# Kernel tuning notes

Hardware: AMD Instinct MI355X
Metric: run time of the kernel (lower is better)

## Reference

```python
import jax, jax.numpy as jnp
import numpy as np

BN_EPS = 1e-5

def _bn_relu(x, gamma, beta):
    # training-mode BatchNorm1d: biased batch stats over (B, N) per channel
    mean = x.mean(axis=(0, 2), keepdims=True)
    var = x.var(axis=(0, 2), keepdims=True)
    xn = (x - mean) * jax.lax.rsqrt(var + BN_EPS)
    return jax.nn.relu(xn * gamma[None, :, None] + beta[None, :, None])


def setup_inputs() -> dict:
    key = jax.random.key(0)
    ks = jax.random.split(key, 12)
    B, n1, n2, c1, c2 = 16, 4096, 1024, 128, 256
    in_ch, mlp = c1 + c2, [256, 128]
    xyz1 = jax.random.uniform(ks[0], (B, n1, 3), dtype=jnp.float32)
    xyz2 = jax.random.uniform(ks[1], (B, n2, 3), dtype=jnp.float32)
    feat1 = jax.random.normal(ks[2], (B, c1, n1), dtype=jnp.float32)
    feat2 = jax.random.normal(ks[3], (B, c2, n2), dtype=jnp.float32)
    # Conv1d(k=1) weights as (out, in) matrices; kaiming-ish scale
    w0 = jax.random.normal(ks[4], (mlp[0], in_ch), dtype=jnp.float32) / np.sqrt(in_ch)
    b0 = jnp.zeros((mlp[0],), jnp.float32)
    g0 = jnp.ones((mlp[0],), jnp.float32)
    be0 = jnp.zeros((mlp[0],), jnp.float32)
    w1 = jax.random.normal(ks[5], (mlp[1], mlp[0]), dtype=jnp.float32) / np.sqrt(mlp[0])
    b1 = jnp.zeros((mlp[1],), jnp.float32)
    g1 = jnp.ones((mlp[1],), jnp.float32)
    be1 = jnp.zeros((mlp[1],), jnp.float32)
    return {"xyz1": xyz1, "xyz2": xyz2, "feat1": feat1, "feat2": feat2,
            "w0": w0, "b0": b0, "g0": g0, "be0": be0,
            "w1": w1, "b1": b1, "g1": g1, "be1": be1}


def reference(xyz1, xyz2, feat1, feat2, w0, b0, g0, be0, w1, b1, g1, be1):
    # three_nn_interpolate: squared pairwise dists (B, n1, n2)
    d = jnp.sum((xyz1[:, :, None, :] - xyz2[:, None, :, :]) ** 2, axis=-1)
    neg_d3, idx3 = jax.lax.top_k(-d, 3)          # 3 smallest dists
    d3 = -neg_d3                                  # (B, n1, 3)
    w = 1.0 / (d3 + 1e-8)
    w = w / jnp.sum(w, axis=-1, keepdims=True)
    # gather feat2 at knn indices: (B, c2, n1, 3)
    gathered = jnp.take_along_axis(feat2[:, :, None, :], idx3[:, None, :, :], axis=3)
    interp = jnp.sum(gathered * w[:, None, :, :], axis=-1)  # (B, c2, n1)

    x = jnp.concatenate([feat1, interp], axis=1)            # (B, c1+c2, n1)
    x = _bn_relu(jnp.einsum('oc,bcn->bon', w0, x) + b0[None, :, None], g0, be0)
    x = _bn_relu(jnp.einsum('oc,bcn->bon', w1, x) + b1[None, :, None], g1, be1)
    return x
```

## Files before the change

kernel.cpp:

```cpp
#include <hip/hip_runtime.h>
#include <hip/hip_bf16.h>

typedef unsigned short u16;
typedef __attribute__((ext_vector_type(8))) __bf16 bf16x8;
typedef __attribute__((ext_vector_type(4))) float floatx4;

#define B_   16
#define N1_  4096
#define N2_  1024
#define C1_  128
#define C2_  256
#define CIN_ 384
#define CM_  256
#define CO_  128

__device__ __forceinline__ u16 f2bf(float f) {
  unsigned u = __float_as_uint(f);
  u = (u + 0x7fffu + ((u >> 16) & 1u)) >> 16;
  return (u16)u;
}
__device__ __forceinline__ float bf2f(u16 h) {
  return __uint_as_float(((unsigned)h) << 16);
}

union U128 { uint4 u; bf16x8 v; u16 s[8]; };

__device__ __forceinline__ bf16x8 ldfrag(const u16* p) {
  U128 x; x.u = *(const uint4*)p; return x.v;
}
__device__ __forceinline__ uint4 pack8(const u16* h) {
  uint4 u;
  u.x = (unsigned)h[0] | ((unsigned)h[1] << 16);
  u.y = (unsigned)h[2] | ((unsigned)h[3] << 16);
  u.z = (unsigned)h[4] | ((unsigned)h[5] << 16);
  u.w = (unsigned)h[6] | ((unsigned)h[7] << 16);
  return u;
}


__global__ __launch_bounds__(256) void knn_part_kernel(
    const float* __restrict__ xyz1, const float* __restrict__ xyz2,
    float* __restrict__ pd, int* __restrict__ pi,
    const float* __restrict__ w0, const float* __restrict__ w1,
    u16* __restrict__ w0b, u16* __restrict__ w1b)
{
  __shared__ float4 sp[128];
  int t = threadIdx.x;
  if (blockIdx.x == 16) {
    int item = (blockIdx.y * 8 + blockIdx.z) * 256 + t;
    if (item < 12288) {
      int m = item / 48, kc = item % 48;
      const float* p = w0 + m * CIN_ + kc * 8;
      u16 h8[8];
      #pragma unroll
      for (int j = 0; j < 8; ++j) h8[j] = f2bf(p[j]);
      int mt = m >> 4, col = m & 15, kt = kc >> 2, quad = kc & 3;
      *(uint4*)(w0b + ((mt*12 + kt)*512 + (quad*16 + col)*8)) = pack8(h8);
    } else if (item < 16384) {
      int i2 = item - 12288;
      int m = i2 >> 5, kc = i2 & 31;
      const float* p = w1 + m * CM_ + kc * 8;
      u16 h8[8];
      #pragma unroll
      for (int j = 0; j < 8; ++j) h8[j] = f2bf(p[j]);
      int mt = m >> 4, col = m & 15, kt = kc >> 2, quad = kc & 3;
      *(uint4*)(w1b + ((mt*8 + kt)*512 + (quad*16 + col)*8)) = pack8(h8);
    }
    return;
  }
  int b = blockIdx.y, chunk = blockIdx.z;
  const float* p2 = xyz2 + ((size_t)b * N2_ + chunk * 128) * 3;
  if (t < 128) sp[t] = make_float4(p2[t*3], p2[t*3+1], p2[t*3+2], 0.f);
  __syncthreads();
  int i = blockIdx.x * 256 + t;
  const float* p1 = xyz1 + ((size_t)b * N1_ + i) * 3;
  float x = p1[0], y = p1[1], z = p1[2];
  float d0 = 1e30f, d1 = 1e30f, d2 = 1e30f;
  int i0 = 0, i1 = 0, i2 = 0;
  int jb = chunk * 128;
  #pragma unroll 4
  for (int j = 0; j < 128; ++j) {
    float4 p = sp[j];
    float dx = x - p.x, dy = y - p.y, dz = z - p.z;
    float d = dx*dx + dy*dy + dz*dz;
    if (d < d2) {
      int jj = jb + j;
      if (d < d0)      { d2=d1; i2=i1; d1=d0; i1=i0; d0=d; i0=jj; }
      else if (d < d1) { d2=d1; i2=i1; d1=d;  i1=jj; }
      else             { d2=d;  i2=jj; }
    }
  }
  int o = chunk*65536 + b*4096 + i;
  pd[o] = d0; pd[o + 524288] = d1; pd[o + 1048576] = d2;
  pi[o] = i0; pi[o + 524288] = i1; pi[o + 1048576] = i2;
}

__global__ __launch_bounds__(256) void knn_merge_kernel(
    const float* __restrict__ pd, const int* __restrict__ pi,
    int* __restrict__ idx_out, float* __restrict__ w_out)
{
  int p = blockIdx.x * 256 + threadIdx.x;
  float d0 = 1e30f, d1 = 1e30f, d2 = 1e30f;
  int i0 = 0, i1 = 0, i2 = 0;
  #pragma unroll
  for (int c = 0; c < 8; ++c) {
    int o = c*65536 + p;
    #pragma unroll
    for (int k = 0; k < 3; ++k) {
      float d = pd[o + k*524288];
      int ix = pi[o + k*524288];
      if (d < d2) {
        if (d < d0)      { d2=d1; i2=i1; d1=d0; i1=i0; d0=d; i0=ix; }
        else if (d < d1) { d2=d1; i2=i1; d1=d;  i1=ix; }
        else             { d2=d;  i2=ix; }
      }
    }
  }
  float w0 = 1.f/(d0+1e-8f), w1 = 1.f/(d1+1e-8f), w2 = 1.f/(d2+1e-8f);
  float inv = 1.f/(w0+w1+w2);
  idx_out[p]          = i0;
  idx_out[p +  65536] = i1;
  idx_out[p + 131072] = i2;
  w_out[p]            = w0*inv;
  w_out[p +  65536]   = w1*inv;
  w_out[p + 131072]   = w2*inv;
}

__global__ __launch_bounds__(256) void tr2_kernel(
    const float* __restrict__ feat2, u16* __restrict__ feat2Tb)
{
  __shared__ float sA[64][257];
  int b = blockIdx.y;
  int n0 = blockIdx.x * 64;
  int t = threadIdx.x;
  #pragma unroll
  for (int j = 0; j < 16; ++j) {
    int flat4 = t + j * 256;
    int c = flat4 >> 4, nn4 = (flat4 & 15) * 4;
    float4 v = *(const float4*)(feat2 + ((size_t)b*C2_ + c)*N2_ + n0 + nn4);
    sA[nn4+0][c] = v.x; sA[nn4+1][c] = v.y; sA[nn4+2][c] = v.z; sA[nn4+3][c] = v.w;
  }
  __syncthreads();
  int nn = t & 63, chunk = t >> 6;
  u16* dst = feat2Tb + ((size_t)b*N2_ + n0 + nn)*C2_ + chunk*64;
  #pragma unroll
  for (int g = 0; g < 8; ++g) {
    u16 h8[8];
    #pragma unroll
    for (int j = 0; j < 8; ++j) h8[j] = f2bf(sA[nn][chunk*64 + g*8 + j]);
    *(uint4*)(dst + g*8) = pack8(h8);
  }
}

__global__ __launch_bounds__(256) void prep_fused_kernel(
    const float* __restrict__ feat1, const u16* __restrict__ feat2Tb,
    const int* __restrict__ idx_in, const float* __restrict__ w_in,
    u16* __restrict__ xcatT)
{
  __shared__ float sA[64][133];
  int b = blockIdx.y;
  int t = threadIdx.x;
  if (blockIdx.x < 64) {
    int n0 = blockIdx.x * 64;
    #pragma unroll
    for (int j = 0; j < 8; ++j) {
      int flat4 = t + j * 256;
      int c = flat4 >> 4, nn4 = (flat4 & 15) * 4;
      float4 v = *(const float4*)(feat1 + ((size_t)b*C1_ + c)*N1_ + n0 + nn4);
      sA[nn4+0][c] = v.x; sA[nn4+1][c] = v.y; sA[nn4+2][c] = v.z; sA[nn4+3][c] = v.w;
    }
    __syncthreads();
    int nn = t & 63, chunk = t >> 6;
    int n = n0 + nn, nt = n >> 4, col = n & 15;
    u16* tb = xcatT + ((size_t)b*256 + nt)*12*512;
    #pragma unroll
    for (int g = 0; g < 4; ++g) {
      int c0 = chunk*32 + g*8;
      u16 h8[8];
      #pragma unroll
      for (int j = 0; j < 8; ++j) h8[j] = f2bf(sA[nn][c0 + j]);
      *(uint4*)(tb + (size_t)chunk*512 + (g*16 + col)*8) = pack8(h8);
    }
  } else {
    int p0 = (blockIdx.x - 64) * 64;
    int seg = t & 31;
    int pl  = t >> 5;
    #pragma unroll 2
    for (int pass = 0; pass < 8; ++pass) {
      int n = p0 + pass*8 + pl;
      int base = b*N1_ + n;
      int i0 = idx_in[base], i1 = idx_in[base + 65536], i2 = idx_in[base + 131072];
      float w0 = w_in[base], w1 = w_in[base + 65536], w2 = w_in[base + 131072];
      const u16* fb = feat2Tb + (size_t)b*N2_*C2_ + seg*8;
      U128 a, c, d;
      a.u = *(const uint4*)(fb + (size_t)i0*C2_);
      c.u = *(const uint4*)(fb + (size_t)i1*C2_);
      d.u = *(const uint4*)(fb + (size_t)i2*C2_);
      u16 h8[8];
      #pragma unroll
      for (int j = 0; j < 8; ++j)
        h8[j] = f2bf(w0*bf2f(a.s[j]) + w1*bf2f(c.s[j]) + w2*bf2f(d.s[j]));
      int nt = n >> 4, col = n & 15;
      int kt = 4 + (seg >> 2), quad = seg & 3;
      *(uint4*)(xcatT + (((size_t)b*256 + nt)*12 + kt)*512 + (quad*16 + col)*8) = pack8(h8);
    }
  }
}

__global__ __launch_bounds__(256) void gemm1_mfma(
    const u16* __restrict__ xcatT, const u16* __restrict__ w0b,
    const float* __restrict__ b0p, u16* __restrict__ y0T,
    float* __restrict__ p0)
{
  __shared__ float ps[4][64][2];
  int t = threadIdx.x;
  int wave = t >> 6, lane = t & 63;
  int col = lane & 15, quad = lane >> 4;
  int wm = wave >> 1, wn = wave & 1;
  int b = blockIdx.y;
  int mtb = blockIdx.z*8 + wm*4;
  int ntb = blockIdx.x*8 + wn*4;

  const u16* ap = w0b + lane*8;
  const u16* bp = xcatT + ((size_t)(b*256 + ntb)*12)*512 + lane*8;

  floatx4 acc[4][4] = {};
  bf16x8 af[4], bf[4], afn[4], bfn[4];
  #pragma unroll
  for (int i = 0; i < 4; ++i) {
    af[i] = ldfrag(ap + (size_t)((mtb+i)*12)*512);
    bf[i] = ldfrag(bp + (size_t)(i*12)*512);
  }
  #pragma unroll 1
  for (int kt = 1; kt < 12; ++kt) {
    #pragma unroll
    for (int i = 0; i < 4; ++i) afn[i] = ldfrag(ap + (size_t)((mtb+i)*12 + kt)*512);
    #pragma unroll
    for (int i = 0; i < 4; ++i) bfn[i] = ldfrag(bp + (size_t)(i*12 + kt)*512);
    #pragma unroll
    for (int mt = 0; mt < 4; ++mt)
      #pragma unroll
      for (int nt = 0; nt < 4; ++nt)
        acc[mt][nt] = __builtin_amdgcn_mfma_f32_16x16x32_bf16(af[mt], bf[nt], acc[mt][nt], 0, 0, 0);
    #pragma unroll
    for (int i = 0; i < 4; ++i) { af[i] = afn[i]; bf[i] = bfn[i]; }
  }
  #pragma unroll
  for (int mt = 0; mt < 4; ++mt)
    #pragma unroll
    for (int nt = 0; nt < 4; ++nt)
      acc[mt][nt] = __builtin_amdgcn_mfma_f32_16x16x32_bf16(af[mt], bf[nt], acc[mt][nt], 0, 0, 0);

  int m0 = blockIdx.z*128 + wm*64;
  #pragma unroll
  for (int mt = 0; mt < 4; ++mt) {
    float4 bias4 = *(const float4*)(b0p + m0 + mt*16 + quad*4);
    float bia[4] = {bias4.x, bias4.y, bias4.z, bias4.w};
    int kt_out = (m0 >> 5) + (mt >> 1);
    int quad_out = ((mt & 1) << 1) | (quad >> 1);
    int j0 = (quad & 1) * 4;
    float s[4] = {}, q[4] = {};
    #pragma unroll
    for (int nt = 0; nt < 4; ++nt) {
      int nt_g = ntb + nt;
      u16 h[4];
      #pragma unroll
      for (int r = 0; r < 4; ++r) {
        float v = acc[mt][nt][r] + bia[r];
        u16 hh = f2bf(v);
        float vr = bf2f(hh);
        h[r] = hh; s[r] += vr; q[r] += vr*vr;
      }
      *(ushort4*)(y0T + (((size_t)b*256 + nt_g)*8 + kt_out)*512 + (quad_out*16 + col)*8 + j0)
          = make_ushort4(h[0], h[1], h[2], h[3]);
    }
    #pragma unroll
    for (int r = 0; r < 4; ++r) {
      float ss = s[r], qq = q[r];
      #pragma unroll
      for (int msk = 1; msk < 16; msk <<= 1) { ss += __shfl_xor(ss, msk); qq += __shfl_xor(qq, msk); }
      if (col == 0) {
        ps[wave][mt*16 + quad*4 + r][0] = ss;
        ps[wave][mt*16 + quad*4 + r][1] = qq;
      }
    }
  }
  __syncthreads();
  {
    int c = t >> 1, k = t & 1;
    int wbase = (c >> 6) * 2, ch = c & 63;
    float v = ps[wbase][ch][k] + ps[wbase+1][ch][k];
    size_t l = (size_t)blockIdx.z*512 + blockIdx.y*32 + blockIdx.x;
    p0[l*256 + t] = v;
  }
}

__global__ __launch_bounds__(256) void stats_kernel(
    const float* __restrict__ p, const float* __restrict__ g,
    const float* __restrict__ be, float* __restrict__ scale,
    float* __restrict__ shift, int half_split)
{
  int c = blockIdx.x, t = threadIdx.x;
  size_t base = half_split ? ((size_t)(c >> 7) * 512 * 256 + (size_t)(c & 127) * 2)
                           : ((size_t)c * 2);
  float s = 0.f, q = 0.f;
  #pragma unroll
  for (int i = 0; i < 2; ++i) {
    float2 v = *(const float2*)(p + base + (size_t)(t + i*256) * 256);
    s += v.x; q += v.y;
  }
  #pragma unroll
  for (int m = 1; m < 64; m <<= 1) { s += __shfl_xor(s, m); q += __shfl_xor(q, m); }
  __shared__ float2 red[4];
  if ((t & 63) == 0) red[t >> 6] = make_float2(s, q);
  __syncthreads();
  if (t == 0) {
    float ss = red[0].x + red[1].x + red[2].x + red[3].x;
    float qq = red[0].y + red[1].y + red[2].y + red[3].y;
    float mu  = ss * (1.f/65536.f);
    float var = qq * (1.f/65536.f) - mu*mu;
    float a = g[c] * rsqrtf(var + 1e-5f);
    scale[c] = a; shift[c] = be[c] - mu*a;
  }
}

__global__ __launch_bounds__(256) void gemm2_mfma(
    const u16* __restrict__ y0T, const u16* __restrict__ w1b,
    const float* __restrict__ b1p,
    const float* __restrict__ scale0, const float* __restrict__ shift0,
    float* __restrict__ out, float* __restrict__ p1)
{
  __shared__ float a0s[CM_], bb0s[CM_];
  __shared__ float ps[4][64][2];
  int t = threadIdx.x;
  a0s[t] = scale0[t]; bb0s[t] = shift0[t];
  __syncthreads();
  int wave = t >> 6, lane = t & 63;
  int col = lane & 15, quad = lane >> 4;
  int wm = wave >> 1, wn = wave & 1;
  int b = blockIdx.y;
  int mtb = wm*4;
  int ntb = blockIdx.x*8 + wn*4;

  const u16* ap = w1b + lane*8;
  const u16* bp = y0T + ((size_t)(b*256 + ntb)*8)*512 + lane*8;

  floatx4 acc[4][4] = {};
  bf16x8 af[4], afn[4];
  U128 braw[4], brawn[4];
  #pragma unroll
  for (int i = 0; i < 4; ++i) {
    af[i] = ldfrag(ap + (size_t)((mtb+i)*8)*512);
    braw[i].u = *(const uint4*)(bp + (size_t)(i*8)*512);
  }
  #pragma unroll 1
  for (int kt = 1; kt < 8; ++kt) {
    #pragma unroll
    for (int i = 0; i < 4; ++i) afn[i] = ldfrag(ap + (size_t)((mtb+i)*8 + kt)*512);
    #pragma unroll
    for (int i = 0; i < 4; ++i) brawn[i].u = *(const uint4*)(bp + (size_t)(i*8 + kt)*512);
    int c0 = (kt-1)*32 + quad*8;
    float4 av0 = *(const float4*)&a0s[c0], av1 = *(const float4*)&a0s[c0+4];
    float4 bv0 = *(const float4*)&bb0s[c0], bv1 = *(const float4*)&bb0s[c0+4];
    float av[8] = {av0.x,av0.y,av0.z,av0.w,av1.x,av1.y,av1.z,av1.w};
    float bv[8] = {bv0.x,bv0.y,bv0.z,bv0.w,bv1.x,bv1.y,bv1.z,bv1.w};
    bf16x8 bfv[4];
    #pragma unroll
    for (int i = 0; i < 4; ++i) {
      u16 h8[8];
      #pragma unroll
      for (int j = 0; j < 8; ++j)
        h8[j] = f2bf(fmaxf(fmaf(bf2f(braw[i].s[j]), av[j], bv[j]), 0.f));
      U128 x; x.u = pack8(h8); bfv[i] = x.v;
    }
    #pragma unroll
    for (int mt = 0; mt < 4; ++mt)
      #pragma unroll
      for (int nt = 0; nt < 4; ++nt)
        acc[mt][nt] = __builtin_amdgcn_mfma_f32_16x16x32_bf16(af[mt], bfv[nt], acc[mt][nt], 0, 0, 0);
    #pragma unroll
    for (int i = 0; i < 4; ++i) { af[i] = afn[i]; braw[i] = brawn[i]; }
  }
  {
    int c0 = 7*32 + quad*8;
    float4 av0 = *(const float4*)&a0s[c0], av1 = *(const float4*)&a0s[c0+4];
    float4 bv0 = *(const float4*)&bb0s[c0], bv1 = *(const float4*)&bb0s[c0+4];
    float av[8] = {av0.x,av0.y,av0.z,av0.w,av1.x,av1.y,av1.z,av1.w};
    float bv[8] = {bv0.x,bv0.y,bv0.z,bv0.w,bv1.x,bv1.y,bv1.z,bv1.w};
    bf16x8 bfv[4];
    #pragma unroll
    for (int i = 0; i < 4; ++i) {
      u16 h8[8];
      #pragma unroll
      for (int j = 0; j < 8; ++j)
        h8[j] = f2bf(fmaxf(fmaf(bf2f(braw[i].s[j]), av[j], bv[j]), 0.f));
      U128 x; x.u = pack8(h8); bfv[i] = x.v;
    }
    #pragma unroll
    for (int mt = 0; mt < 4; ++mt)
      #pragma unroll
      for (int nt = 0; nt < 4; ++nt)
        acc[mt][nt] = __builtin_amdgcn_mfma_f32_16x16x32_bf16(af[mt], bfv[nt], acc[mt][nt], 0, 0, 0);
  }

  int m0 = wm*64;
  int n0 = blockIdx.x*128 + wn*64;
  #pragma unroll
  for (int mt = 0; mt < 4; ++mt) {
    float4 bias4 = *(const float4*)(b1p + m0 + mt*16 + quad*4);
    float bia[4] = {bias4.x, bias4.y, bias4.z, bias4.w};
    float s[4] = {}, q[4] = {};
    #pragma unroll
    for (int nt = 0; nt < 4; ++nt) {
      int n = n0 + nt*16 + col;
      #pragma unroll
      for (int r = 0; r < 4; ++r) {
        float v = acc[mt][nt][r] + bia[r];
        out[((size_t)b*CO_ + m0 + mt*16 + quad*4 + r)*N1_ + n] = v;
        s[r] += v; q[r] += v*v;
      }
    }
    #pragma unroll
    for (int r = 0; r < 4; ++r) {
      float ss = s[r], qq = q[r];
      #pragma unroll
      for (int msk = 1; msk < 16; msk <<= 1) { ss += __shfl_xor(ss, msk); qq += __shfl_xor(qq, msk); }
      if (col == 0) {
        ps[wave][mt*16 + quad*4 + r][0] = ss;
        ps[wave][mt*16 + quad*4 + r][1] = qq;
      }
    }
  }
  __syncthreads();
  {
    int c = t >> 1, k = t & 1;
    int wbase = (c >> 6) * 2, ch = c & 63;
    float v = ps[wbase][ch][k] + ps[wbase+1][ch][k];
    size_t l = (size_t)blockIdx.y*32 + blockIdx.x;
    p1[l*256 + t] = v;
  }
}

__global__ __launch_bounds__(256) void bnrelu_kernel(
    float* __restrict__ out, const float* __restrict__ scale1, const float* __restrict__ shift1)
{
  int idx = blockIdx.x * 256 + threadIdx.x;
  int c = (idx >> 10) & (CO_ - 1);
  float a = scale1[c];
  float bb = shift1[c];
  float4 v = ((const float4*)out)[idx];
  v.x = fmaxf(fmaf(v.x, a, bb), 0.f);
  v.y = fmaxf(fmaf(v.y, a, bb), 0.f);
  v.z = fmaxf(fmaf(v.z, a, bb), 0.f);
  v.w = fmaxf(fmaf(v.w, a, bb), 0.f);
  ((float4*)out)[idx] = v;
}

extern "C" void kernel_launch(void* const* d_in, const int* in_sizes, int n_in,
                              void* d_out, int out_size, void* d_ws, size_t ws_size,
                              hipStream_t stream)
{
  const float* xyz1  = (const float*)d_in[0];
  const float* xyz2  = (const float*)d_in[1];
  const float* feat1 = (const float*)d_in[2];
  const float* feat2 = (const float*)d_in[3];
  const float* w0    = (const float*)d_in[4];
  const float* b0    = (const float*)d_in[5];
  const float* g0    = (const float*)d_in[6];
  const float* be0   = (const float*)d_in[7];
  const float* w1    = (const float*)d_in[8];
  const float* b1    = (const float*)d_in[9];
  const float* g1    = (const float*)d_in[10];
  const float* be1   = (const float*)d_in[11];
  float* out = (float*)d_out;
  char* ws = (char*)d_ws;

  u16*   xcatT   = (u16*)ws;
  float* knn_pd  = (float*)ws;
  int*   knn_pi  = (int*)(ws + 6291456);
  u16*   y0T     = (u16*)(ws + 50331648);
  u16*   feat2Tb = (u16*)(ws + 50331648);
  u16*   w0b     = (u16*)(ws + 83886080);
  u16*   w1b     = (u16*)(ws + 84082688);
  int*   idx_buf = (int*)(ws + 84148224);
  float* w_buf   = (float*)(ws + 84934656);
  float* p0      = (float*)(ws + 85721088);
  float* p1      = (float*)(ws + 86769664);
  float* scale0  = (float*)(ws + 87293952);
  float* shift0  = scale0 + 256;
  float* scale1  = scale0 + 512;
  float* shift1  = scale0 + 640;

  knn_part_kernel <<<dim3(17,16,8),   256, 0, stream>>>(xyz1, xyz2, knn_pd, knn_pi, w0, w1, w0b, w1b);
  knn_merge_kernel<<<256,             256, 0, stream>>>(knn_pd, knn_pi, idx_buf, w_buf);
  tr2_kernel      <<<dim3(16,16),     256, 0, stream>>>(feat2, feat2Tb);
  prep_fused_kernel<<<dim3(128,16),   256, 0, stream>>>(feat1, feat2Tb, idx_buf, w_buf, xcatT);
  gemm1_mfma      <<<dim3(32,16,2),   256, 0, stream>>>(xcatT, w0b, b0, y0T, p0);
  stats_kernel    <<<256,             256, 0, stream>>>(p0, g0, be0, scale0, shift0, 1);
  gemm2_mfma      <<<dim3(32,16),     256, 0, stream>>>(y0T, w1b, b1, scale0, shift0, out, p1);
  stats_kernel    <<<128,             256, 0, stream>>>(p1, g1, be1, scale1, shift1, 0);
  bnrelu_kernel   <<<8192,            256, 0, stream>>>(out, scale1, shift1);
}
```

Measured before the change: 250.9 us.

## Stage gemm1 fragments through double-buffered LDS via global_load_lds

The first MFMA GEMM now loads the A (weight) and B (activation) tiles for each k-step cooperatively into a double-buffered shared-memory buffer, using direct global-to-LDS loads. Each wave then reads its fragments from LDS. Before, every wave fetched its own fragments straight from global memory, so each fragment was fetched by two waves. The change is meant to halve global/L2 traffic for gemm1 and overlap the next tile's fetch with the current MFMAs. In exchange it adds a block-wide barrier every k-step and depends on the 16-byte global_load_lds path.

```diff
diff --git a/kernel.cpp b/kernel.cpp
--- a/kernel.cpp
+++ b/kernel.cpp
@@ -212,44 +212,56 @@
     const float* __restrict__ b0p, u16* __restrict__ y0T,
     float* __restrict__ p0)
 {
+  __shared__ u16 sbuf[2][16][512];
   __shared__ float ps[4][64][2];
   int t = threadIdx.x;
   int wave = t >> 6, lane = t & 63;
   int col = lane & 15, quad = lane >> 4;
   int wm = wave >> 1, wn = wave & 1;
   int b = blockIdx.y;
-  int mtb = blockIdx.z*8 + wm*4;
-  int ntb = blockIdx.x*8 + wn*4;
-
-  const u16* ap = w0b + lane*8;
-  const u16* bp = xcatT + ((size_t)(b*256 + ntb)*12)*512 + lane*8;
+  int mtb8 = blockIdx.z * 8;
+  int ntb8 = blockIdx.x * 8;
+
+  const u16* asrc = w0b + (size_t)mtb8 * 12 * 512 + lane * 8;
+  const u16* bsrc = xcatT + ((size_t)(b * 256 + ntb8) * 12) * 512 + lane * 8;
+  const u16* stage_base = (wave < 2) ? (asrc + (size_t)(wave * 4) * 12 * 512)
+                                     : (bsrc + (size_t)((wave - 2) * 4) * 12 * 512);
 
   floatx4 acc[4][4] = {};
-  bf16x8 af[4], bf[4], afn[4], bfn[4];
-  #pragma unroll
-  for (int i = 0; i < 4; ++i) {
-    af[i] = ldfrag(ap + (size_t)((mtb+i)*12)*512);
-    bf[i] = ldfrag(bp + (size_t)(i*12)*512);
-  }
+
+  #pragma unroll
+  for (int i = 0; i < 4; ++i)
+    __builtin_amdgcn_global_load_lds(
+        (const __attribute__((address_space(1))) void*)(stage_base + (size_t)i * 12 * 512),
+        (__attribute__((address_space(3))) void*)(&sbuf[0][wave * 4 + i][0]),
+        16, 0, 0);
+  __syncthreads();
+
+  int cur = 0;
   #pragma unroll 1
-  for (int kt = 1; kt < 12; ++kt) {
-    #pragma unroll
-    for (int i = 0; i < 4; ++i) afn[i] = ldfrag(ap + (size_t)((mtb+i)*12 + kt)*512);
-    #pragma unroll
-    for (int i = 0; i < 4; ++i) bfn[i] = ldfrag(bp + (size_t)(i*12 + kt)*512);
+  for (int kt = 0; kt < 12; ++kt) {
+    if (kt < 11) {
+      #pragma unroll
+      for (int i = 0; i < 4; ++i)
+        __builtin_amdgcn_global_load_lds(
+            (const __attribute__((address_space(1))) void*)(stage_base + (size_t)(i * 12 + kt + 1) * 512),
+            (__attribute__((address_space(3))) void*)(&sbuf[cur ^ 1][wave * 4 + i][0]),
+            16, 0, 0);
+    }
+    bf16x8 af[4], bfr[4];
+    #pragma unroll
+    for (int i = 0; i < 4; ++i) {
+      af[i]  = ldfrag(&sbuf[cur][wm * 4 + i][lane * 8]);
+      bfr[i] = ldfrag(&sbuf[cur][8 + wn * 4 + i][lane * 8]);
+    }
     #pragma unroll
     for (int mt = 0; mt < 4; ++mt)
       #pragma unroll
       for (int nt = 0; nt < 4; ++nt)
-        acc[mt][nt] = __builtin_amdgcn_mfma_f32_16x16x32_bf16(af[mt], bf[nt], acc[mt][nt], 0, 0, 0);
-    #pragma unroll
-    for (int i = 0; i < 4; ++i) { af[i] = afn[i]; bf[i] = bfn[i]; }
-  }
-  #pragma unroll
-  for (int mt = 0; mt < 4; ++mt)
-    #pragma unroll
-    for (int nt = 0; nt < 4; ++nt)
-      acc[mt][nt] = __builtin_amdgcn_mfma_f32_16x16x32_bf16(af[mt], bf[nt], acc[mt][nt], 0, 0, 0);
+        acc[mt][nt] = __builtin_amdgcn_mfma_f32_16x16x32_bf16(af[mt], bfr[nt], acc[mt][nt], 0, 0, 0);
+    __syncthreads();
+    cur ^= 1;
+  }
 
   int m0 = blockIdx.z*128 + wm*64;
   #pragma unroll
@@ -260,6 +272,7 @@
     int quad_out = ((mt & 1) << 1) | (quad >> 1);
     int j0 = (quad & 1) * 4;
     float s[4] = {}, q[4] = {};
+    int ntb = ntb8 + wn*4;
     #pragma unroll
     for (int nt = 0; nt < 4; ++nt) {
       int nt_g = ntb + nt;
```

Result: no change. 253.1 us (+0.9%).
